# Kernel optimization log

Measured on AMD Instinct MI355X. Metric: run time of the kernel, lower is better.

The kernel has to match this reference:

```python
import jax, jax.numpy as jnp
import numpy as np

N_NODES = 100000
N_EDGES = 800000
DIM = 64
HEADS = 4
HEAD_DIM = DIM // HEADS  # 16
ALPHA = 0.1
K_ITERS = 8  # fixed-point iterations approximating the implicit/CG solve


def setup_inputs() -> dict:
    key = jax.random.key(0)
    ks = jax.random.split(key, 7)
    x = jax.random.normal(ks[0], (N_NODES, DIM), dtype=jnp.float32)
    edge_index = jax.random.randint(ks[1], (2, N_EDGES), 0, N_NODES, dtype=jnp.int64)
    edge_attr = jax.random.normal(ks[2], (N_EDGES, DIM), dtype=jnp.float32)
    s = 1.0 / np.sqrt(DIM)
    Wq = jax.random.normal(ks[3], (DIM, DIM), dtype=jnp.float32) * s
    Wk = jax.random.normal(ks[4], (DIM, DIM), dtype=jnp.float32) * s
    Wv = jax.random.normal(ks[5], (DIM, DIM), dtype=jnp.float32) * s
    We = jax.random.normal(ks[6], (DIM, DIM), dtype=jnp.float32) * s
    return {"x": x, "edge_index": edge_index, "edge_attr": edge_attr,
            "Wq": Wq, "Wk": Wk, "Wv": Wv, "We": We}


def _mapr(x, edge_index, edge_attr, Wq, Wk, Wv, We):
    N = x.shape[0]
    src, dst = edge_index[0], edge_index[1]
    q = (x @ Wq).reshape(N, HEADS, HEAD_DIM)
    k = (x @ Wk).reshape(N, HEADS, HEAD_DIM)
    v = (x @ Wv).reshape(N, HEADS, HEAD_DIM)
    e = (edge_attr @ We).reshape(-1, HEADS, HEAD_DIM)
    # per-edge multi-head dot attention logits, edge features modulate keys
    logits = jnp.sum(q[dst] * (k[src] + e), axis=-1) / np.sqrt(HEAD_DIM)  # [E,H]
    # segment softmax over incoming edges of each dst node
    m = jax.ops.segment_max(logits, dst, num_segments=N)  # [N,H]
    ex = jnp.exp(logits - m[dst])
    denom = jax.ops.segment_sum(ex, dst, num_segments=N)  # [N,H]
    att = ex / (denom[dst] + 1e-16)  # [E,H]
    # implicit propagation: fixed-point solve of z = alpha*v + (1-alpha) * A_att z
    def step(z, _):
        msg = att[:, :, None] * z[src]                       # [E,H,D]
        agg = jax.ops.segment_sum(msg, dst, num_segments=N)  # [N,H,D]
        return ALPHA * v + (1.0 - ALPHA) * agg, None
    z, _ = jax.lax.scan(step, v, None, length=K_ITERS)
    return z.reshape(N, DIM)


def reference(x, edge_index, edge_attr, Wq, Wk, Wv, We):
    h = _mapr(x, edge_index, edge_attr, Wq, Wk, Wv, We)
    h = jax.nn.relu(h)  # act; dropout is identity in eval mode
    return x + h        # residual
```

## Files before the change

### kernel.cpp

```cpp
#include <hip/hip_runtime.h>
#include <hip/hip_fp16.h>
#include <cstdint>
#include <cstddef>

#define NN 100000
#define NE 800000
#define DIM 64
#define HEADS 4
#define HEAD_DIM 16
#define ALPHA 0.1f
#define K_ITERS 8
#define NBLK 391

__device__ __forceinline__ unsigned short f2bf(float f) {
    unsigned int x = __float_as_uint(f);
    unsigned int r = (x + 0x7fffu + ((x >> 16) & 1u)) >> 16;
    return (unsigned short)r;
}
__device__ __forceinline__ float bf_lo(unsigned int p) { return __uint_as_float(p << 16); }
__device__ __forceinline__ float bf_hi(unsigned int p) { return __uint_as_float(p & 0xffff0000u); }

__device__ __forceinline__ float2 h2f(unsigned int v) {
    __half2 h = *(__half2*)&v;
    return __half22float2(h);
}
__device__ __forceinline__ unsigned int f2h2(float a, float b) {
    __half2 h = __floats2half2_rn(a, b);
    return *(unsigned int*)&h;
}
__device__ __forceinline__ float dot8h(uint4 a, uint4 b) {
    float2 a0 = h2f(a.x), b0 = h2f(b.x);
    float2 a1 = h2f(a.y), b1 = h2f(b.y);
    float2 a2 = h2f(a.z), b2 = h2f(b.z);
    float2 a3 = h2f(a.w), b3 = h2f(b.w);
    return a0.x * b0.x + a0.y * b0.y + a1.x * b1.x + a1.y * b1.y
         + a2.x * b2.x + a2.y * b2.y + a3.x * b3.x + a3.y * b3.y;
}

#define ACC8(a, V) { float2 t_; \
    t_ = h2f((V).x); m[0] += (a) * t_.x; m[1] += (a) * t_.y; \
    t_ = h2f((V).y); m[2] += (a) * t_.x; m[3] += (a) * t_.y; \
    t_ = h2f((V).z); m[4] += (a) * t_.x; m[5] += (a) * t_.y; \
    t_ = h2f((V).w); m[6] += (a) * t_.x; m[7] += (a) * t_.y; }

__global__ void qkv_kernel(const float* __restrict__ x,
                           const float* __restrict__ Wq,
                           const float* __restrict__ Wk,
                           const float* __restrict__ Wv,
                           const float* __restrict__ We,
                           __half* __restrict__ qh, __half* __restrict__ kh,
                           __half* __restrict__ vh,
                           unsigned short* __restrict__ u) {
    __shared__ float sW[3][DIM * DIM];
    __shared__ float sWe[DIM * 65];
    __shared__ float sx[4][DIM];
    __shared__ float sq[4][DIM];
    int tid = threadIdx.x;
    for (int i = tid; i < DIM * DIM; i += 256) {
        sW[0][i] = Wq[i]; sW[1][i] = Wk[i]; sW[2][i] = Wv[i];
        sWe[(i >> 6) * 65 + (i & 63)] = We[i];
    }
    int node = blockIdx.x * 4 + (tid >> 6);
    int c = tid & 63;
    int slot = tid >> 6;
    if (node < NN) sx[slot][c] = x[(size_t)node * DIM + c];
    __syncthreads();
    if (node >= NN) return;
    const float* xr = sx[slot];
    float aq = 0.f, ak = 0.f, av = 0.f;
    #pragma unroll 8
    for (int d = 0; d < DIM; ++d) {
        float xv = xr[d];
        aq += xv * sW[0][d * DIM + c];
        ak += xv * sW[1][d * DIM + c];
        av += xv * sW[2][d * DIM + c];
    }
    aq *= 0.25f;
    size_t o = (size_t)node * DIM + c;
    qh[o] = __float2half(aq);
    kh[o] = __float2half(ak);
    vh[o] = __float2half(av);
    sq[slot][c] = aq;
    __syncthreads();
    const float* qr = sq[slot];
    #pragma unroll
    for (int h = 0; h < HEADS; ++h) {
        float acc = 0.f;
        #pragma unroll
        for (int d = 0; d < HEAD_DIM; ++d)
            acc += sWe[c * 65 + h * HEAD_DIM + d] * qr[h * HEAD_DIM + d];
        u[(size_t)node * 256 + h * 64 + c] = f2bf(acc);
    }
}

__global__ void init_kernel(float* __restrict__ denom, int* __restrict__ deg) {
    int i = blockIdx.x * 256 + threadIdx.x;
    if (i < NN * HEADS) denom[i] = 0.f;
    if (i < NN) deg[i] = 0;
}

__global__ void deg_kernel(const int* __restrict__ ei, int* __restrict__ deg) {
    int e = blockIdx.x * 256 + threadIdx.x;
    if (e >= NE) return;
    atomicAdd(&deg[ei[NE + e]], 1);
}

__global__ void blocksum_kernel(const int* __restrict__ deg, int* __restrict__ bsum) {
    int t = threadIdx.x, b = blockIdx.x;
    int idx = b * 256 + t;
    int v = (idx < NN) ? deg[idx] : 0;
    #pragma unroll
    for (int off = 32; off > 0; off >>= 1) v += __shfl_down(v, off);
    __shared__ int wsum[4];
    if ((t & 63) == 0) wsum[t >> 6] = v;
    __syncthreads();
    if (t == 0) bsum[b] = wsum[0] + wsum[1] + wsum[2] + wsum[3];
}

__global__ void bscan_kernel(const int* __restrict__ bsum, int* __restrict__ boff) {
    __shared__ int s[512];
    int t = threadIdx.x;
    int v = (t < NBLK) ? bsum[t] : 0;
    s[t] = v;
    __syncthreads();
    for (int off = 1; off < 512; off <<= 1) {
        int u = (t >= off) ? s[t - off] : 0;
        __syncthreads();
        s[t] += u;
        __syncthreads();
    }
    if (t < NBLK) boff[t] = s[t] - v;
}

__global__ void rowptr_kernel(const int* __restrict__ deg, const int* __restrict__ boff,
                              int* __restrict__ row_ptr, int* __restrict__ cursor) {
    __shared__ int s[256];
    int t = threadIdx.x, b = blockIdx.x;
    int idx = b * 256 + t;
    int v = (idx < NN) ? deg[idx] : 0;
    s[t] = v;
    __syncthreads();
    for (int off = 1; off < 256; off <<= 1) {
        int u = (t >= off) ? s[t - off] : 0;
        __syncthreads();
        s[t] += u;
        __syncthreads();
    }
    if (idx < NN) {
        int ex = boff[b] + s[t] - v;
        row_ptr[idx] = ex;
        cursor[idx] = ex;
    }
    if (idx == 0) row_ptr[NN] = NE;
}

__global__ void scatter_kernel(const int* __restrict__ ei,
                               int* __restrict__ cursor,
                               int* __restrict__ csr_src,
                               int* __restrict__ csr_e,
                               int* __restrict__ csr_dst) {
    int e = blockIdx.x * 256 + threadIdx.x;
    if (e >= NE) return;
    int src = ei[e], dst = ei[NE + e];
    int pos = atomicAdd(&cursor[dst], 1);
    csr_src[pos] = src;
    csr_e[pos] = e;
    csr_dst[pos] = dst;
}

__global__ void logits_csr_kernel(const __half* __restrict__ qh,
                                  const __half* __restrict__ kh,
                                  const float* __restrict__ edge_attr,
                                  const unsigned short* __restrict__ u,
                                  const int* __restrict__ csr_src,
                                  const int* __restrict__ csr_e,
                                  const int* __restrict__ csr_dst,
                                  __half* __restrict__ att,
                                  float* __restrict__ denom) {
    int idx = blockIdx.x * 256 + threadIdx.x;
    if (idx >= NE * HEADS) return;
    int j = idx >> 2, h = idx & 3;
    int src = csr_src[j], dst = csr_dst[j], e = csr_e[j];
    const float4* attr4 = (const float4*)edge_attr + (size_t)e * 16;
    const uint4* u4 = (const uint4*)u + (size_t)dst * 32 + h * 8;
    float au = 0.f;
    #pragma unroll
    for (int i = 0; i < 8; ++i) {
        uint4 up = u4[i];
        float4 a0 = attr4[2 * i];
        float4 a1 = attr4[2 * i + 1];
        au += a0.x * bf_lo(up.x) + a0.y * bf_hi(up.x)
            + a0.z * bf_lo(up.y) + a0.w * bf_hi(up.y)
            + a1.x * bf_lo(up.z) + a1.y * bf_hi(up.z)
            + a1.z * bf_lo(up.w) + a1.w * bf_hi(up.w);
    }
    const uint4* qq = (const uint4*)qh + (size_t)dst * 8 + h * 2;
    const uint4* kk = (const uint4*)kh + (size_t)src * 8 + h * 2;
    float qk = dot8h(qq[0], kk[0]) + dot8h(qq[1], kk[1]);
    float ex = __expf(qk + au);
    att[idx] = __float2half(ex);
    atomicAdd(&denom[dst * HEADS + h], ex);
}

__global__ void prop_csr_kernel(const __half* __restrict__ zin,
                                const __half* __restrict__ vh,
                                const __half* __restrict__ att,
                                const int* __restrict__ csr_src,
                                const int* __restrict__ row_ptr,
                                const float* __restrict__ denom,
                                __half* __restrict__ zout) {
    int gid = blockIdx.x * 256 + threadIdx.x;
    int node = gid >> 3;
    if (node >= NN) return;
    int l = gid & 7;
    int head = l >> 1;
    const uint4* z4 = (const uint4*)zin;
    float m[8];
    #pragma unroll
    for (int i = 0; i < 8; ++i) m[i] = 0.f;
    int beg = row_ptr[node], end = row_ptr[node + 1];
    int j = beg;
    for (; j + 4 <= end; j += 4) {
        int s0 = csr_src[j], s1 = csr_src[j + 1], s2 = csr_src[j + 2], s3 = csr_src[j + 3];
        float a0 = __half2float(att[4 * j + head]);
        float a1 = __half2float(att[4 * j + 4 + head]);
        float a2 = __half2float(att[4 * j + 8 + head]);
        float a3 = __half2float(att[4 * j + 12 + head]);
        uint4 z0 = z4[(size_t)s0 * 8 + l];
        uint4 z1 = z4[(size_t)s1 * 8 + l];
        uint4 z2 = z4[(size_t)s2 * 8 + l];
        uint4 z3 = z4[(size_t)s3 * 8 + l];
        ACC8(a0, z0); ACC8(a1, z1); ACC8(a2, z2); ACC8(a3, z3);
    }
    for (; j < end; ++j) {
        int s = csr_src[j];
        float a = __half2float(att[4 * j + head]);
        uint4 zl = z4[(size_t)s * 8 + l];
        ACC8(a, zl);
    }
    float r = 0.9f / (denom[node * HEADS + head] + 1e-16f);
    uint4 vv = ((const uint4*)vh)[(size_t)node * 8 + l];
    float2 v0 = h2f(vv.x), v1 = h2f(vv.y), v2 = h2f(vv.z), v3 = h2f(vv.w);
    uint4 o;
    o.x = f2h2(ALPHA * v0.x + r * m[0], ALPHA * v0.y + r * m[1]);
    o.y = f2h2(ALPHA * v1.x + r * m[2], ALPHA * v1.y + r * m[3]);
    o.z = f2h2(ALPHA * v2.x + r * m[4], ALPHA * v2.y + r * m[5]);
    o.w = f2h2(ALPHA * v3.x + r * m[6], ALPHA * v3.y + r * m[7]);
    ((uint4*)zout)[(size_t)node * 8 + l] = o;
}

__global__ void prop_out_kernel(const __half* __restrict__ zin,
                                const __half* __restrict__ vh,
                                const __half* __restrict__ att,
                                const int* __restrict__ csr_src,
                                const int* __restrict__ row_ptr,
                                const float* __restrict__ denom,
                                const float* __restrict__ x,
                                float* __restrict__ out) {
    int gid = blockIdx.x * 256 + threadIdx.x;
    int node = gid >> 3;
    if (node >= NN) return;
    int l = gid & 7;
    int head = l >> 1;
    const uint4* z4 = (const uint4*)zin;
    float m[8];
    #pragma unroll
    for (int i = 0; i < 8; ++i) m[i] = 0.f;
    int beg = row_ptr[node], end = row_ptr[node + 1];
    int j = beg;
    for (; j + 4 <= end; j += 4) {
        int s0 = csr_src[j], s1 = csr_src[j + 1], s2 = csr_src[j + 2], s3 = csr_src[j + 3];
        float a0 = __half2float(att[4 * j + head]);
        float a1 = __half2float(att[4 * j + 4 + head]);
        float a2 = __half2float(att[4 * j + 8 + head]);
        float a3 = __half2float(att[4 * j + 12 + head]);
        uint4 z0 = z4[(size_t)s0 * 8 + l];
        uint4 z1 = z4[(size_t)s1 * 8 + l];
        uint4 z2 = z4[(size_t)s2 * 8 + l];
        uint4 z3 = z4[(size_t)s3 * 8 + l];
        ACC8(a0, z0); ACC8(a1, z1); ACC8(a2, z2); ACC8(a3, z3);
    }
    for (; j < end; ++j) {
        int s = csr_src[j];
        float a = __half2float(att[4 * j + head]);
        uint4 zl = z4[(size_t)s * 8 + l];
        ACC8(a, zl);
    }
    float r = 0.9f / (denom[node * HEADS + head] + 1e-16f);
    uint4 vv = ((const uint4*)vh)[(size_t)node * 8 + l];
    float2 v0 = h2f(vv.x), v1 = h2f(vv.y), v2 = h2f(vv.z), v3 = h2f(vv.w);
    float zf[8] = { ALPHA * v0.x + r * m[0], ALPHA * v0.y + r * m[1],
                    ALPHA * v1.x + r * m[2], ALPHA * v1.y + r * m[3],
                    ALPHA * v2.x + r * m[4], ALPHA * v2.y + r * m[5],
                    ALPHA * v3.x + r * m[6], ALPHA * v3.y + r * m[7] };
    const float4* x4 = (const float4*)x + (size_t)node * 16 + l * 2;
    float4 xa = x4[0], xb = x4[1];
    float4 oa, ob;
    oa.x = xa.x + fmaxf(zf[0], 0.f); oa.y = xa.y + fmaxf(zf[1], 0.f);
    oa.z = xa.z + fmaxf(zf[2], 0.f); oa.w = xa.w + fmaxf(zf[3], 0.f);
    ob.x = xb.x + fmaxf(zf[4], 0.f); ob.y = xb.y + fmaxf(zf[5], 0.f);
    ob.z = xb.z + fmaxf(zf[6], 0.f); ob.w = xb.w + fmaxf(zf[7], 0.f);
    float4* o4 = (float4*)out + (size_t)node * 16 + l * 2;
    o4[0] = oa; o4[1] = ob;
}

extern "C" void kernel_launch(void* const* d_in, const int* in_sizes, int n_in,
                              void* d_out, int out_size, void* d_ws, size_t ws_size,
                              hipStream_t stream) {
    const float* x         = (const float*)d_in[0];
    const int*   ei        = (const int*)d_in[1];
    const float* edge_attr = (const float*)d_in[2];
    const float* Wq        = (const float*)d_in[3];
    const float* Wk        = (const float*)d_in[4];
    const float* Wv        = (const float*)d_in[5];
    const float* We        = (const float*)d_in[6];
    float* out = (float*)d_out;

    __half* qh = (__half*)d_ws;
    __half* kh = qh + (size_t)NN * DIM;
    __half* vh = kh + (size_t)NN * DIM;
    unsigned short* u = (unsigned short*)(vh + (size_t)NN * DIM);
    __half* zha = (__half*)(u + (size_t)NN * 256);
    __half* zhb = zha + (size_t)NN * DIM;
    __half* att = zhb + (size_t)NN * DIM;
    float* denom = (float*)(att + (size_t)NE * HEADS);
    int* deg     = (int*)(denom + (size_t)NN * HEADS);
    int* bsum    = deg + NN;
    int* boff    = bsum + NBLK;
    int* row_ptr = boff + NBLK;
    int* cursor  = row_ptr + NN + 1;
    int* csr_src = cursor + NN;
    int* csr_e   = csr_src + NE;
    int* csr_dst = csr_e + NE;

    hipLaunchKernelGGL(qkv_kernel, dim3(NN / 4), dim3(256), 0, stream,
                       x, Wq, Wk, Wv, We, qh, kh, vh, u);
    hipLaunchKernelGGL(init_kernel, dim3((NN * HEADS + 255) / 256), dim3(256), 0, stream,
                       denom, deg);
    hipLaunchKernelGGL(deg_kernel, dim3((NE + 255) / 256), dim3(256), 0, stream,
                       ei, deg);
    hipLaunchKernelGGL(blocksum_kernel, dim3(NBLK), dim3(256), 0, stream,
                       deg, bsum);
    hipLaunchKernelGGL(bscan_kernel, dim3(1), dim3(512), 0, stream,
                       bsum, boff);
    hipLaunchKernelGGL(rowptr_kernel, dim3(NBLK), dim3(256), 0, stream,
                       deg, boff, row_ptr, cursor);
    hipLaunchKernelGGL(scatter_kernel, dim3((NE + 255) / 256), dim3(256), 0, stream,
                       ei, cursor, csr_src, csr_e, csr_dst);
    hipLaunchKernelGGL(logits_csr_kernel, dim3(NE * HEADS / 256), dim3(256), 0, stream,
                       qh, kh, edge_attr, u, csr_src, csr_e, csr_dst, att, denom);

    const __half* zin = vh;
    __half* zout = zha;
    for (int it = 0; it < K_ITERS - 1; ++it) {
        hipLaunchKernelGGL(prop_csr_kernel, dim3((NN * 8 + 255) / 256), dim3(256), 0, stream,
                           zin, vh, att, csr_src, row_ptr, denom, zout);
        zin = zout;
        zout = (zout == zha) ? zhb : zha;
    }
    hipLaunchKernelGGL(prop_out_kernel, dim3((NN * 8 + 255) / 256), dim3(256), 0, stream,
                       zin, vh, att, csr_src, row_ptr, denom, x, out);
}
```

Baseline: 874.4 us.

## Compute QKV and edge-key projection with bf16 MFMA instructions

Replaces the scalar FP32 shared-memory QKV projection kernel with one built on 16x16x32 bf16 MFMA, handling 64 nodes per block instead of 4. The q·We product (u) is also done with MFMA, using masked per-head B fragments. This removes the per-block reload of all four weight matrices into LDS and the scalar FMA loops. In exchange, x, W and q are rounded to bf16 before multiplication, which lowers precision, and weights are read straight from global memory with strided per-lane loads.

```diff
diff --git a/kernel.cpp b/kernel.cpp
--- a/kernel.cpp
+++ b/kernel.cpp
@@ -12,6 +12,9 @@
 #define K_ITERS 8
 #define NBLK 391
 
+typedef short bf16x8 __attribute__((ext_vector_type(8)));
+typedef float f32x4 __attribute__((ext_vector_type(4)));
+
 __device__ __forceinline__ unsigned short f2bf(float f) {
     unsigned int x = __float_as_uint(f);
     unsigned int r = (x + 0x7fffu + ((x >> 16) & 1u)) >> 16;
@@ -43,53 +46,87 @@
     t_ = h2f((V).z); m[4] += (a) * t_.x; m[5] += (a) * t_.y; \
     t_ = h2f((V).w); m[6] += (a) * t_.x; m[7] += (a) * t_.y; }
 
-__global__ void qkv_kernel(const float* __restrict__ x,
-                           const float* __restrict__ Wq,
-                           const float* __restrict__ Wk,
-                           const float* __restrict__ Wv,
-                           const float* __restrict__ We,
-                           __half* __restrict__ qh, __half* __restrict__ kh,
-                           __half* __restrict__ vh,
-                           unsigned short* __restrict__ u) {
-    __shared__ float sW[3][DIM * DIM];
-    __shared__ float sWe[DIM * 65];
-    __shared__ float sx[4][DIM];
-    __shared__ float sq[4][DIM];
+__global__ __launch_bounds__(256) void qkv_mfma_kernel(
+    const float* __restrict__ x,
+    const float* __restrict__ Wq, const float* __restrict__ Wk,
+    const float* __restrict__ Wv, const float* __restrict__ We,
+    __half* __restrict__ qh, __half* __restrict__ kh, __half* __restrict__ vh,
+    unsigned short* __restrict__ u)
+{
+    __shared__ unsigned short sq[64 * 72];
     int tid = threadIdx.x;
-    for (int i = tid; i < DIM * DIM; i += 256) {
-        sW[0][i] = Wq[i]; sW[1][i] = Wk[i]; sW[2][i] = Wv[i];
-        sWe[(i >> 6) * 65 + (i & 63)] = We[i];
-    }
-    int node = blockIdx.x * 4 + (tid >> 6);
-    int c = tid & 63;
-    int slot = tid >> 6;
-    if (node < NN) sx[slot][c] = x[(size_t)node * DIM + c];
+    int w = tid >> 6;
+    int lane = tid & 63;
+    int m16 = lane & 15;
+    int quad = lane >> 4;
+    int node = blockIdx.x * 64 + w * 16 + m16;
+    int nodeC = node < NN ? node : NN - 1;
+
+    bf16x8 afrag[2];
+    #pragma unroll
+    for (int kk = 0; kk < 2; ++kk) {
+        const float* xr = x + (size_t)nodeC * DIM + kk * 32 + quad * 8;
+        #pragma unroll
+        for (int j = 0; j < 8; ++j) afrag[kk][j] = (short)f2bf(xr[j]);
+    }
+
+    const float* Ws[3] = {Wq, Wk, Wv};
+    __half* outs[3] = {qh, kh, vh};
+
+    #pragma unroll
+    for (int mtx = 0; mtx < 3; ++mtx) {
+        const float* W = Ws[mtx];
+        #pragma unroll
+        for (int n0 = 0; n0 < 64; n0 += 16) {
+            int col = n0 + m16;
+            f32x4 acc = {0.f, 0.f, 0.f, 0.f};
+            #pragma unroll
+            for (int kk = 0; kk < 2; ++kk) {
+                bf16x8 bfrag;
+                #pragma unroll
+                for (int j = 0; j < 8; ++j)
+                    bfrag[j] = (short)f2bf(W[(kk * 32 + quad * 8 + j) * DIM + col]);
+                acc = __builtin_amdgcn_mfma_f32_16x16x32_bf16(afrag[kk], bfrag, acc, 0, 0, 0);
+            }
+            if (mtx == 0) {
+                #pragma unroll
+                for (int r = 0; r < 4; ++r) acc[r] *= 0.25f;
+            }
+            #pragma unroll
+            for (int r = 0; r < 4; ++r) {
+                int rl = w * 16 + quad * 4 + r;
+                int gnode = blockIdx.x * 64 + rl;
+                if (mtx == 0) sq[rl * 72 + col] = f2bf(acc[r]);
+                if (gnode < NN) outs[mtx][(size_t)gnode * DIM + col] = __float2half(acc[r]);
+            }
+        }
+    }
     __syncthreads();
-    if (node >= NN) return;
-    const float* xr = sx[slot];
-    float aq = 0.f, ak = 0.f, av = 0.f;
-    #pragma unroll 8
-    for (int d = 0; d < DIM; ++d) {
-        float xv = xr[d];
-        aq += xv * sW[0][d * DIM + c];
-        ak += xv * sW[1][d * DIM + c];
-        av += xv * sW[2][d * DIM + c];
-    }
-    aq *= 0.25f;
-    size_t o = (size_t)node * DIM + c;
-    qh[o] = __float2half(aq);
-    kh[o] = __float2half(ak);
-    vh[o] = __float2half(av);
-    sq[slot][c] = aq;
-    __syncthreads();
-    const float* qr = sq[slot];
+
     #pragma unroll
     for (int h = 0; h < HEADS; ++h) {
-        float acc = 0.f;
+        int kk = h >> 1;
+        bf16x8 aq;
+        const unsigned short* sr = &sq[(w * 16 + m16) * 72 + kk * 32 + quad * 8];
         #pragma unroll
-        for (int d = 0; d < HEAD_DIM; ++d)
-            acc += sWe[c * 65 + h * HEAD_DIM + d] * qr[h * HEAD_DIM + d];
-        u[(size_t)node * 256 + h * 64 + c] = f2bf(acc);
+        for (int j = 0; j < 8; ++j) aq[j] = (short)sr[j];
+        #pragma unroll
+        for (int c0 = 0; c0 < 64; c0 += 16) {
+            int c = c0 + m16;
+            bf16x8 bfrag;
+            #pragma unroll
+            for (int j = 0; j < 8; ++j) {
+                int k = kk * 32 + quad * 8 + j;
+                bfrag[j] = ((k >> 4) == h) ? (short)f2bf(We[c * DIM + k]) : (short)0;
+            }
+            f32x4 acc = {0.f, 0.f, 0.f, 0.f};
+            acc = __builtin_amdgcn_mfma_f32_16x16x32_bf16(aq, bfrag, acc, 0, 0, 0);
+            #pragma unroll
+            for (int r = 0; r < 4; ++r) {
+                int gnode = blockIdx.x * 64 + w * 16 + quad * 4 + r;
+                if (gnode < NN) u[(size_t)gnode * 256 + h * 64 + c] = f2bf(acc[r]);
+            }
+        }
     }
 }
 
@@ -333,7 +370,7 @@
     int* csr_e   = csr_src + NE;
     int* csr_dst = csr_e + NE;
 
-    hipLaunchKernelGGL(qkv_kernel, dim3(NN / 4), dim3(256), 0, stream,
+    hipLaunchKernelGGL(qkv_mfma_kernel, dim3((NN + 63) / 64), dim3(256), 0, stream,
                        x, Wq, Wk, Wv, We, qh, kh, vh, u);
     hipLaunchKernelGGL(init_kernel, dim3((NN * HEADS + 255) / 256), dim3(256), 0, stream,
                        denom, deg);
```

New measurement: 735.5 us. -15.9%, faster.
